# Kernel tuning notes

Hardware: AMD Instinct MI355X
Metric: run time of the kernel (lower is better)

## Reference

```python
import jax, jax.numpy as jnp
import numpy as np

N = 100000      # nodes
E = 6400000     # directed edges (avg degree 64)
NDIM = 128      # input feature dim
H = 8           # hidden_dim (module default)


def _lin_init(key, fan_in, fan_out):
    # torch nn.Linear-style uniform init (exact init values don't affect correctness testing)
    k1, k2 = jax.random.split(key)
    s = 1.0 / np.sqrt(fan_in)
    W = jax.random.uniform(k1, (fan_in, fan_out), jnp.float32, -s, s)
    b = jax.random.uniform(k2, (fan_out,), jnp.float32, -s, s)
    return W, b


def setup_inputs() -> dict:
    key = jax.random.key(0)
    ks = jax.random.split(key, 8)
    x = jax.random.normal(ks[0], (N, NDIM), jnp.float32)
    edge_index = jax.random.randint(ks[1], (2, E), 0, N, dtype=jnp.int64)
    W1, b1 = _lin_init(ks[2], NDIM, H)
    W2, b2 = _lin_init(ks[3], H, H)
    W3, b3 = _lin_init(ks[4], H, H)
    Wp, bp = _lin_init(ks[5], H, 1)
    Wv, bv = _lin_init(ks[6], H, 1)
    return dict(x=x, edge_index=edge_index,
                W1=W1, b1=b1, W2=W2, b2=b2, W3=W3, b3=b3,
                Wp=Wp, bp=bp, Wv=Wv, bv=bv)


def reference(x, edge_index, W1, b1, W2, b2, W3, b3, Wp, bp, Wv, bv):
    n = x.shape[0]
    # GCNConv: add self-loops, symmetric normalization deg^{-1/2} A_hat deg^{-1/2}
    loop = jnp.arange(n, dtype=edge_index.dtype)
    row = jnp.concatenate([edge_index[0], loop])  # source nodes
    col = jnp.concatenate([edge_index[1], loop])  # target nodes
    deg = jax.ops.segment_sum(jnp.ones(row.shape[0], jnp.float32), col, num_segments=n)
    dis = jnp.where(deg > 0, jax.lax.rsqrt(deg), 0.0)
    norm = dis[row] * dis[col]  # [E+N]

    def gcn_conv(h, W, b):
        h = h @ W                                   # [n, out] linear transform first
        msg = h[row] * norm[:, None]                # gather + per-edge scale
        return jax.ops.segment_sum(msg, col, num_segments=n) + b  # scatter-add + bias

    h = jax.nn.relu(gcn_conv(x, W1, b1))
    h = jax.nn.relu(gcn_conv(h, W2, b2))
    h = jax.nn.relu(gcn_conv(h, W3, b3))

    mean_val = jnp.mean(h, axis=0, keepdims=True)   # global_mean_pool, single graph
    proba = h @ Wp + bp                             # [n, 1]
    value = mean_val @ Wv + bv                      # [1, 1]
    return proba, value
```

## Files before the change

kernel.cpp:

```cpp
#include <hip/hip_runtime.h>
#include <hip/hip_fp16.h>
#include <math.h>


static constexpr int HDIM = 8;
#define EPB_B 16
#define NBMAX 128
#define NS 4
#define BSH 10
#define BSZ 1024
#define STG 18432
#define CAP 73728

__global__ void k_zero(int* __restrict__ deg, int* __restrict__ bcur,
                       int n, int nbuck) {
    int i = blockIdx.x * 256 + threadIdx.x;
    if (i < n) deg[i] = 0;
    if (i < nbuck) bcur[i] = 0;
}

__global__ void k_bucket(const int* __restrict__ row, const int* __restrict__ col,
                         int E, int nbuck, int* __restrict__ bcur,
                         unsigned* __restrict__ bedge) {
    __shared__ int lcol[256 * EPB_B];
    __shared__ int lrow[256 * EPB_B];
    __shared__ int lcnt[NBMAX];
    __shared__ int lbase[NBMAX];
    int t = threadIdx.x;
    if (t < nbuck) lcnt[t] = 0;
    int base = blockIdx.x * (256 * EPB_B);
    int m = E - base; if (m > 256 * EPB_B) m = 256 * EPB_B;
    for (int q = t; q < m; q += 256) {
        lcol[q] = col[base + q];
        lrow[q] = row[base + q];
    }
    __syncthreads();
    for (int q = t; q < m; q += 256) atomicAdd(&lcnt[lcol[q] >> BSH], 1);
    __syncthreads();
    if (t < nbuck) {
        int c = lcnt[t];
        lbase[t] = c ? atomicAdd(&bcur[t], c) : 0;
        lcnt[t] = 0;
    }
    __syncthreads();
    for (int q = t; q < m; q += 256) {
        int c = lcol[q];
        int b = c >> BSH;
        int r = atomicAdd(&lcnt[b], 1);
        bedge[(size_t)b * CAP + lbase[b] + r] =
            ((unsigned)lrow[q] << BSH) | (unsigned)(c & (BSZ - 1));
    }
}

__global__ void k_sortchunk(const int* __restrict__ blen, unsigned* __restrict__ bedge,
                            int2* __restrict__ rc, int* __restrict__ deg) {
    __shared__ int hist[BSZ];
    __shared__ int basec[BSZ];
    __shared__ int stag[STG];
    int t = threadIdx.x;
    int b = blockIdx.x / NS, s = blockIdx.x % NS;
    long long s0 = (long long)b * CAP;
    int len = blen[b];
    int lo = (int)(s0 + (long long)len * s / NS);
    int hi = (int)(s0 + (long long)len * (s + 1) / NS);
    int m = hi - lo;
    for (int q = t; q < BSZ; q += 256) hist[q] = 0;
    __syncthreads();
    for (int p = lo + t; p < hi; p += 256) atomicAdd(&hist[bedge[p] & (BSZ - 1)], 1);
    __syncthreads();
    int v0 = hist[t * 4], v1 = hist[t * 4 + 1], v2 = hist[t * 4 + 2], v3 = hist[t * 4 + 3];
    int sum = v0 + v1 + v2 + v3;
    stag[t] = sum;
    __syncthreads();
    for (int d = 1; d < 256; d <<= 1) {
        int x = stag[t];
        int a = (t >= d) ? stag[t - d] : 0;
        __syncthreads();
        stag[t] = x + a;
        __syncthreads();
    }
    int run = (t == 0) ? 0 : stag[t - 1];
    basec[t * 4] = run;
    basec[t * 4 + 1] = run + v0;
    basec[t * 4 + 2] = run + v0 + v1;
    basec[t * 4 + 3] = run + v0 + v1 + v2;
    __syncthreads();
    size_t obase = (size_t)blockIdx.x * BSZ;
    int gb = b << BSH;
#pragma unroll
    for (int q = 0; q < 4; ++q) {
        int lc = t * 4 + q;
        int h = hist[lc];
        rc[obase + lc] = make_int2(lo + basec[lc], h);
        if (h) atomicAdd(&deg[gb + lc], h);
    }
    __syncthreads();
    for (int p = lo + t; p < hi; p += 256) {
        unsigned e = bedge[p];
        int pos = atomicAdd(&basec[e & (BSZ - 1)], 1);
        stag[pos] = (int)(e >> BSH);
    }
    __syncthreads();
    for (int p = t; p < m; p += 256) bedge[lo + p] = (unsigned)stag[p];
}

__global__ void k_proj1(const float* __restrict__ x, const float* __restrict__ W1,
                        const int* __restrict__ deg, float* __restrict__ dis,
                        __half* __restrict__ g, int n) {
    __shared__ float Ws[32 * 36];
    const float4* Ws4 = (const float4*)Ws;
    for (int t = threadIdx.x; t < 1024; t += 256) {
        int c = t >> 5, rem = t & 31, j = rem >> 2, r = rem & 3;
        Ws[c * 36 + j * 4 + r] = W1[(c * 4 + r) * 8 + j];
    }
    __syncthreads();
    int t4 = blockIdx.x * blockDim.x + threadIdx.x;
    int i = t4 >> 2, sub = t4 & 3;
    if (i >= n) return;
    const float4* x4 = (const float4*)x;
    float a[HDIM] = {0, 0, 0, 0, 0, 0, 0, 0};
#pragma unroll
    for (int iter = 0; iter < 8; ++iter) {
        int c = iter * 4 + sub;
        float4 xv = x4[(size_t)i * 32 + c];
#pragma unroll
        for (int j = 0; j < HDIM; ++j) {
            float4 wv = Ws4[c * 9 + j];
            a[j] += xv.x * wv.x + xv.y * wv.y + xv.z * wv.z + xv.w * wv.w;
        }
    }
#pragma unroll
    for (int j = 0; j < HDIM; ++j) {
        a[j] += __shfl_xor(a[j], 1);
        a[j] += __shfl_xor(a[j], 2);
    }
    float di = rsqrtf((float)(deg[i] + 1));
    if (sub == 2) dis[i] = di;
    if (sub < 2) {
        __half2 h0 = __floats2half2_rn(di * a[sub * 4 + 0], di * a[sub * 4 + 1]);
        __half2 h1 = __floats2half2_rn(di * a[sub * 4 + 2], di * a[sub * 4 + 3]);
        float2 st;
        ((__half2*)&st)[0] = h0;
        ((__half2*)&st)[1] = h1;
        ((float2*)g)[(size_t)i * 2 + sub] = st;
    }
}

#define ACCUM(rv)                                                         \
    {                                                                     \
        const __half2* hp = (const __half2*)&(rv);                        \
        float2 f0 = __half22float2(hp[0]), f1 = __half22float2(hp[1]);    \
        float2 f2 = __half22float2(hp[2]), f3 = __half22float2(hp[3]);    \
        a[0] += f0.x; a[1] += f0.y; a[2] += f1.x; a[3] += f1.y;           \
        a[4] += f2.x; a[5] += f2.y; a[6] += f3.x; a[7] += f3.y;           \
    }

#define GATHER4(r0, r1, r2, r3)                                           \
    {                                                                     \
        float4 rv0 = g4[(size_t)(r0)];                                    \
        float4 rv1 = g4[(size_t)(r1)];                                    \
        float4 rv2 = g4[(size_t)(r2)];                                    \
        float4 rv3 = g4[(size_t)(r3)];                                    \
        ACCUM(rv0); ACCUM(rv1); ACCUM(rv2); ACCUM(rv3);                   \
    }

#define GATHER1(r)                                                        \
    {                                                                     \
        float4 rv = g4[(size_t)(r)];                                      \
        ACCUM(rv);                                                        \
    }

#define GATHER_RANGE(p, e)                                                \
    {                                                                     \
        while (p < e && (p & 3)) { GATHER1(perm[p]); ++p; }               \
        for (; p + 7 < e; p += 8) {                                       \
            int4 ra = *(const int4*)(perm + p);                           \
            int4 rb = *(const int4*)(perm + p + 4);                       \
            GATHER4(ra.x, ra.y, ra.z, ra.w);                              \
            GATHER4(rb.x, rb.y, rb.z, rb.w);                              \
        }                                                                 \
        if (p + 3 < e) {                                                  \
            int4 ra = *(const int4*)(perm + p);                           \
            GATHER4(ra.x, ra.y, ra.z, ra.w);                              \
            p += 4;                                                       \
        }                                                                 \
        for (; p < e; ++p) GATHER1(perm[p]);                              \
    }

__global__ void k_flayer(const int2* __restrict__ rc, const int* __restrict__ perm,
                         const __half* __restrict__ g_in, __half* __restrict__ g_out,
                         const float* __restrict__ dis, const float* __restrict__ bias,
                         const float* __restrict__ Wn, int n) {
    __shared__ float Ws[HDIM * HDIM];
    __shared__ float bs[HDIM];
    int t = threadIdx.x;
    if (t < HDIM * HDIM) Ws[t] = Wn[t];
    if (t < HDIM) bs[t] = bias[t];
    __syncthreads();
    int q = t >> 3, sub = t & 7;
    int run = sub >> 1, half = sub & 1;
    int i = blockIdx.x * 32 + q;
    if (i >= n) return;
    int bkt = i >> BSH, lc = i & (BSZ - 1);
    int2 r2 = rc[((size_t)bkt * NS + run) * BSZ + lc];
    int p = r2.x + ((r2.y * half) >> 1);
    int e = r2.x + ((r2.y * (half + 1)) >> 1);
    const float4* g4 = (const float4*)g_in;
    float a[HDIM] = {0, 0, 0, 0, 0, 0, 0, 0};
    GATHER_RANGE(p, e);
#pragma unroll
    for (int j = 0; j < HDIM; ++j) {
        a[j] += __shfl_xor(a[j], 1);
        a[j] += __shfl_xor(a[j], 2);
        a[j] += __shfl_xor(a[j], 4);
    }
    float di = dis[i];
    float4 sv = g4[(size_t)i];
    const __half2* sp = (const __half2*)&sv;
    float2 s0 = __half22float2(sp[0]), s1 = __half22float2(sp[1]);
    float2 s2 = __half22float2(sp[2]), s3 = __half22float2(sp[3]);
    float h[HDIM];
    h[0] = fmaxf(di * (a[0] + s0.x) + bs[0], 0.0f);
    h[1] = fmaxf(di * (a[1] + s0.y) + bs[1], 0.0f);
    h[2] = fmaxf(di * (a[2] + s1.x) + bs[2], 0.0f);
    h[3] = fmaxf(di * (a[3] + s1.y) + bs[3], 0.0f);
    h[4] = fmaxf(di * (a[4] + s2.x) + bs[4], 0.0f);
    h[5] = fmaxf(di * (a[5] + s2.y) + bs[5], 0.0f);
    h[6] = fmaxf(di * (a[6] + s3.x) + bs[6], 0.0f);
    h[7] = fmaxf(di * (a[7] + s3.y) + bs[7], 0.0f);
    if (sub < 4) {
        int j0 = sub * 2;
        float gn0 = 0.0f, gn1 = 0.0f;
#pragma unroll
        for (int k = 0; k < HDIM; ++k) {
            gn0 += h[k] * Ws[k * HDIM + j0];
            gn1 += h[k] * Ws[k * HDIM + j0 + 1];
        }
        ((__half2*)g_out)[(size_t)i * 4 + sub] = __floats2half2_rn(di * gn0, di * gn1);
    }
}

__global__ void k_flayer3(const int2* __restrict__ rc, const int* __restrict__ perm,
                          const __half* __restrict__ g_in, const float* __restrict__ dis,
                          const float* __restrict__ b3, const float* __restrict__ Wp,
                          const float* __restrict__ bp, float* __restrict__ out,
                          float* __restrict__ partial, int n) {
    __shared__ float red[4][HDIM];
    int t = threadIdx.x;
    int q = t >> 3, sub = t & 7;
    int run = sub >> 1, half = sub & 1;
    int i = blockIdx.x * 32 + q;
    bool valid = i < n;
    const float4* g4 = (const float4*)g_in;
    float a[HDIM] = {0, 0, 0, 0, 0, 0, 0, 0};
    if (valid) {
        int bkt = i >> BSH, lc = i & (BSZ - 1);
        int2 r2 = rc[((size_t)bkt * NS + run) * BSZ + lc];
        int p = r2.x + ((r2.y * half) >> 1);
        int e = r2.x + ((r2.y * (half + 1)) >> 1);
        GATHER_RANGE(p, e);
    }
#pragma unroll
    for (int j = 0; j < HDIM; ++j) {
        a[j] += __shfl_xor(a[j], 1);
        a[j] += __shfl_xor(a[j], 2);
        a[j] += __shfl_xor(a[j], 4);
    }
    float h[HDIM] = {0, 0, 0, 0, 0, 0, 0, 0};
    if (valid) {
        float di = dis[i];
        float4 sv = g4[(size_t)i];
        const __half2* sp = (const __half2*)&sv;
        float2 s0 = __half22float2(sp[0]), s1 = __half22float2(sp[1]);
        float2 s2 = __half22float2(sp[2]), s3 = __half22float2(sp[3]);
        h[0] = fmaxf(di * (a[0] + s0.x) + b3[0], 0.0f);
        h[1] = fmaxf(di * (a[1] + s0.y) + b3[1], 0.0f);
        h[2] = fmaxf(di * (a[2] + s1.x) + b3[2], 0.0f);
        h[3] = fmaxf(di * (a[3] + s1.y) + b3[3], 0.0f);
        h[4] = fmaxf(di * (a[4] + s2.x) + b3[4], 0.0f);
        h[5] = fmaxf(di * (a[5] + s2.y) + b3[5], 0.0f);
        h[6] = fmaxf(di * (a[6] + s3.x) + b3[6], 0.0f);
        h[7] = fmaxf(di * (a[7] + s3.y) + b3[7], 0.0f);
        if (sub == 0) {
            float p2 = bp[0];
#pragma unroll
            for (int j = 0; j < HDIM; ++j) p2 += h[j] * Wp[j];
            out[i] = p2;
        }
    }
    int w = t >> 6, lane = t & 63;
#pragma unroll
    for (int j = 0; j < HDIM; ++j) {
        float sj = (sub == 0) ? h[j] : 0.0f;
#pragma unroll
        for (int o = 32; o > 0; o >>= 1) sj += __shfl_down(sj, o);
        if (lane == 0) red[w][j] = sj;
    }
    __syncthreads();
    if (t < HDIM)
        partial[(size_t)blockIdx.x * HDIM + t] =
            red[0][t] + red[1][t] + red[2][t] + red[3][t];
}

__global__ void k_value(const float* __restrict__ partial, int nblocks,
                        const float* __restrict__ Wv, const float* __restrict__ bv,
                        float* __restrict__ out, int n) {
    __shared__ float red[256];
    int t = threadIdx.x;
    int j = t & 7, c = t >> 3;
    float v = 0.0f;
    for (int b = c; b < nblocks; b += 32) v += partial[(size_t)b * HDIM + j];
    red[t] = v;
    __syncthreads();
    for (int d = 128; d >= 8; d >>= 1) {
        if (t < d) red[t] += red[t + d];
        __syncthreads();
    }
    if (t == 0) {
        float val = bv[0];
        float inv_n = 1.0f / (float)n;
#pragma unroll
        for (int jj = 0; jj < HDIM; ++jj) val += (red[jj] * inv_n) * Wv[jj];
        out[n] = val;
    }
}

extern "C" void kernel_launch(void* const* d_in, const int* in_sizes, int n_in,
                              void* d_out, int out_size, void* d_ws, size_t ws_size,
                              hipStream_t stream) {
    const float* x  = (const float*)d_in[0];
    const int*   ei = (const int*)d_in[1];
    const float* W1 = (const float*)d_in[2];
    const float* b1 = (const float*)d_in[3];
    const float* W2 = (const float*)d_in[4];
    const float* b2 = (const float*)d_in[5];
    const float* W3 = (const float*)d_in[6];
    const float* b3 = (const float*)d_in[7];
    const float* Wp = (const float*)d_in[8];
    const float* bp = (const float*)d_in[9];
    const float* Wv = (const float*)d_in[10];
    const float* bv = (const float*)d_in[11];

    const int n = in_sizes[0] / 128;
    const int E = in_sizes[1] / 2;
    const int* row = ei;
    const int* col = ei + E;
    const int nbuck = (n + BSZ - 1) >> BSH;

    int*      bcur  = (int*)d_ws;
    float*    dis   = (float*)(bcur + 1024);
    int*      deg   = (int*)(dis + n);
    unsigned* bedge = (unsigned*)(deg + n);
    int2*     rc    = (int2*)(bedge + (size_t)nbuck * CAP);
    __half*   g_a   = (__half*)(rc + (size_t)nbuck * NS * BSZ);
    __half*   g_b   = g_a + (size_t)n * HDIM;
    float*    partial = (float*)(g_b + (size_t)n * HDIM);
    int*      perm  = (int*)bedge;

    dim3 blk(256);
    dim3 grid_n4(((size_t)n * 4 + 255) / 256);
    dim3 grid_eb((E + 256 * EPB_B - 1) / (256 * EPB_B));
    dim3 grid_sc(nbuck * NS);
    dim3 grid_f((n + 31) / 32);
    const int nblocks3 = (n + 31) / 32;

    k_zero  <<<dim3((n + 255) / 256), blk, 0, stream>>>(deg, bcur, n, nbuck);
    k_bucket<<<grid_eb, blk, 0, stream>>>(row, col, E, nbuck, bcur, bedge);
    k_sortchunk<<<grid_sc, blk, 0, stream>>>(bcur, bedge, rc, deg);
    k_proj1 <<<grid_n4, blk, 0, stream>>>(x, W1, deg, dis, g_a, n);

    k_flayer<<<grid_f, blk, 0, stream>>>(rc, perm, g_a, g_b, dis, b1, W2, n);
    k_flayer<<<grid_f, blk, 0, stream>>>(rc, perm, g_b, g_a, dis, b2, W3, n);
    k_flayer3<<<grid_f, blk, 0, stream>>>(rc, perm, g_a, dis, b3, Wp, bp,
                                          (float*)d_out, partial, n);
    k_value <<<dim3(1), blk, 0, stream>>>(partial, nblocks3, Wv, bv,
                                          (float*)d_out, n);
}
```

Before: 253.0 us.

## Derive degrees from sort histograms and fold value reduction into last layer

After: 478.6 us. 89.2% more time.

```diff
diff --git a/kernel.cpp b/kernel.cpp
--- a/kernel.cpp
+++ b/kernel.cpp
@@ -12,11 +12,10 @@
 #define STG 18432
 #define CAP 73728
 
-__global__ void k_zero(int* __restrict__ deg, int* __restrict__ bcur,
-                       int n, int nbuck) {
-    int i = blockIdx.x * 256 + threadIdx.x;
-    if (i < n) deg[i] = 0;
+__global__ void k_zero(int* __restrict__ bcur, int* __restrict__ done, int nbuck) {
+    int i = threadIdx.x;
     if (i < nbuck) bcur[i] = 0;
+    if (i == nbuck) *done = 0;
 }
 
 __global__ void k_bucket(const int* __restrict__ row, const int* __restrict__ col,
@@ -53,7 +52,7 @@
 }
 
 __global__ void k_sortchunk(const int* __restrict__ blen, unsigned* __restrict__ bedge,
-                            int2* __restrict__ rc, int* __restrict__ deg) {
+                            int2* __restrict__ rc) {
     __shared__ int hist[BSZ];
     __shared__ int basec[BSZ];
     __shared__ int stag[STG];
@@ -86,13 +85,10 @@
     basec[t * 4 + 3] = run + v0 + v1 + v2;
     __syncthreads();
     size_t obase = (size_t)blockIdx.x * BSZ;
-    int gb = b << BSH;
 #pragma unroll
     for (int q = 0; q < 4; ++q) {
         int lc = t * 4 + q;
-        int h = hist[lc];
-        rc[obase + lc] = make_int2(lo + basec[lc], h);
-        if (h) atomicAdd(&deg[gb + lc], h);
+        rc[obase + lc] = make_int2(lo + basec[lc], hist[lc]);
     }
     __syncthreads();
     for (int p = lo + t; p < hi; p += 256) {
@@ -105,7 +101,7 @@
 }
 
 __global__ void k_proj1(const float* __restrict__ x, const float* __restrict__ W1,
-                        const int* __restrict__ deg, float* __restrict__ dis,
+                        const int2* __restrict__ rc, float* __restrict__ dis,
                         __half* __restrict__ g, int n) {
     __shared__ float Ws[32 * 36];
     const float4* Ws4 = (const float4*)Ws;
@@ -117,6 +113,8 @@
     int t4 = blockIdx.x * blockDim.x + threadIdx.x;
     int i = t4 >> 2, sub = t4 & 3;
     if (i >= n) return;
+    int bkt = i >> BSH, lc = i & (BSZ - 1);
+    int dcnt = rc[((size_t)bkt * NS + sub) * BSZ + lc].y;
     const float4* x4 = (const float4*)x;
     float a[HDIM] = {0, 0, 0, 0, 0, 0, 0, 0};
 #pragma unroll
@@ -129,12 +127,14 @@
             a[j] += xv.x * wv.x + xv.y * wv.y + xv.z * wv.z + xv.w * wv.w;
         }
     }
+    dcnt += __shfl_xor(dcnt, 1);
+    dcnt += __shfl_xor(dcnt, 2);
 #pragma unroll
     for (int j = 0; j < HDIM; ++j) {
         a[j] += __shfl_xor(a[j], 1);
         a[j] += __shfl_xor(a[j], 2);
     }
-    float di = rsqrtf((float)(deg[i] + 1));
+    float di = rsqrtf((float)(dcnt + 1));
     if (sub == 2) dis[i] = di;
     if (sub < 2) {
         __half2 h0 = __floats2half2_rn(di * a[sub * 4 + 0], di * a[sub * 4 + 1]);
@@ -243,8 +243,9 @@
 __global__ void k_flayer3(const int2* __restrict__ rc, const int* __restrict__ perm,
                           const __half* __restrict__ g_in, const float* __restrict__ dis,
                           const float* __restrict__ b3, const float* __restrict__ Wp,
-                          const float* __restrict__ bp, float* __restrict__ out,
-                          float* __restrict__ partial, int n) {
+                          const float* __restrict__ bp, const float* __restrict__ Wv,
+                          const float* __restrict__ bv, float* __restrict__ out,
+                          float* __restrict__ partial, int* __restrict__ done, int n) {
     __shared__ float red[4][HDIM];
     int t = threadIdx.x;
     int q = t >> 3, sub = t & 7;
@@ -300,28 +301,31 @@
     if (t < HDIM)
         partial[(size_t)blockIdx.x * HDIM + t] =
             red[0][t] + red[1][t] + red[2][t] + red[3][t];
-}
-
-__global__ void k_value(const float* __restrict__ partial, int nblocks,
-                        const float* __restrict__ Wv, const float* __restrict__ bv,
-                        float* __restrict__ out, int n) {
-    __shared__ float red[256];
-    int t = threadIdx.x;
-    int j = t & 7, c = t >> 3;
-    float v = 0.0f;
-    for (int b = c; b < nblocks; b += 32) v += partial[(size_t)b * HDIM + j];
-    red[t] = v;
-    __syncthreads();
-    for (int d = 128; d >= 8; d >>= 1) {
-        if (t < d) red[t] += red[t + d];
+    __threadfence();
+    __syncthreads();
+    __shared__ int rank;
+    if (t == 0) rank = atomicAdd(done, 1);
+    __syncthreads();
+    if (rank == gridDim.x - 1) {
+        __threadfence();
+        __shared__ float vred[256];
+        int j = t & 7, c = t >> 3;
+        float v = 0.0f;
+        for (int b = c; b < (int)gridDim.x; b += 32)
+            v += partial[(size_t)b * HDIM + j];
+        vred[t] = v;
         __syncthreads();
-    }
-    if (t == 0) {
-        float val = bv[0];
-        float inv_n = 1.0f / (float)n;
-#pragma unroll
-        for (int jj = 0; jj < HDIM; ++jj) val += (red[jj] * inv_n) * Wv[jj];
-        out[n] = val;
+        for (int d = 128; d >= 8; d >>= 1) {
+            if (t < d) vred[t] += vred[t + d];
+            __syncthreads();
+        }
+        if (t == 0) {
+            float val = bv[0];
+            float inv_n = 1.0f / (float)n;
+#pragma unroll
+            for (int jj = 0; jj < HDIM; ++jj) val += (vred[jj] * inv_n) * Wv[jj];
+            out[n] = val;
+        }
     }
 }
 
@@ -348,9 +352,9 @@
     const int nbuck = (n + BSZ - 1) >> BSH;
 
     int*      bcur  = (int*)d_ws;
+    int*      done  = bcur + 512;
     float*    dis   = (float*)(bcur + 1024);
-    int*      deg   = (int*)(dis + n);
-    unsigned* bedge = (unsigned*)(deg + n);
+    unsigned* bedge = (unsigned*)(dis + n);
     int2*     rc    = (int2*)(bedge + (size_t)nbuck * CAP);
     __half*   g_a   = (__half*)(rc + (size_t)nbuck * NS * BSZ);
     __half*   g_b   = g_a + (size_t)n * HDIM;
@@ -362,17 +366,14 @@
     dim3 grid_eb((E + 256 * EPB_B - 1) / (256 * EPB_B));
     dim3 grid_sc(nbuck * NS);
     dim3 grid_f((n + 31) / 32);
-    const int nblocks3 = (n + 31) / 32;
-
-    k_zero  <<<dim3((n + 255) / 256), blk, 0, stream>>>(deg, bcur, n, nbuck);
+
+    k_zero  <<<dim3(1), dim3(256), 0, stream>>>(bcur, done, nbuck);
     k_bucket<<<grid_eb, blk, 0, stream>>>(row, col, E, nbuck, bcur, bedge);
-    k_sortchunk<<<grid_sc, blk, 0, stream>>>(bcur, bedge, rc, deg);
-    k_proj1 <<<grid_n4, blk, 0, stream>>>(x, W1, deg, dis, g_a, n);
+    k_sortchunk<<<grid_sc, blk, 0, stream>>>(bcur, bedge, rc);
+    k_proj1 <<<grid_n4, blk, 0, stream>>>(x, W1, rc, dis, g_a, n);
 
     k_flayer<<<grid_f, blk, 0, stream>>>(rc, perm, g_a, g_b, dis, b1, W2, n);
     k_flayer<<<grid_f, blk, 0, stream>>>(rc, perm, g_b, g_a, dis, b2, W3, n);
-    k_flayer3<<<grid_f, blk, 0, stream>>>(rc, perm, g_a, dis, b3, Wp, bp,
-                                          (float*)d_out, partial, n);
-    k_value <<<dim3(1), blk, 0, stream>>>(partial, nblocks3, Wv, bv,
-                                          (float*)d_out, n);
-}
+    k_flayer3<<<grid_f, blk, 0, stream>>>(rc, perm, g_a, dis, b3, Wp, bp, Wv, bv,
+                                          (float*)d_out, partial, done, n);
+}
```
